# Performance work log

Hardware: AMD Instinct MI355X
Metric: run time of the kernel (lower is better)

Reference implementation:

```python
import jax, jax.numpy as jnp
import numpy as np

C_S, C_Z, H = 384, 128, 8
HD = C_S // H
EPS = 1e-5

def _layernorm(x, g, b):
    mu = jnp.mean(x, axis=-1, keepdims=True)
    var = jnp.mean((x - mu) ** 2, axis=-1, keepdims=True)
    return (x - mu) * jax.lax.rsqrt(var + EPS) * g + b

def setup_inputs() -> dict:
    key = jax.random.key(0)
    ks = jax.random.split(key, 12)
    B, L = 1, 768
    sc = lambda d: 1.0 / np.sqrt(d)
    return {
        "single": jax.random.normal(ks[0], (B, L, C_S), jnp.float32),
        "pair": jax.random.normal(ks[1], (B, L, L, C_Z), jnp.float32),
        "g_s": jnp.ones((C_S,), jnp.float32),
        "b_s": jnp.zeros((C_S,), jnp.float32),
        "g_z": jnp.ones((C_Z,), jnp.float32),
        "b_z": jnp.zeros((C_Z,), jnp.float32),
        "Wq": jax.random.normal(ks[2], (C_S, C_S), jnp.float32) * sc(C_S),
        "Wk": jax.random.normal(ks[3], (C_S, C_S), jnp.float32) * sc(C_S),
        "Wv": jax.random.normal(ks[4], (C_S, C_S), jnp.float32) * sc(C_S),
        "Wb": jax.random.normal(ks[5], (C_Z, H), jnp.float32) * sc(C_Z),
        "Wo": jax.random.normal(ks[6], (C_S, C_S), jnp.float32) * sc(C_S),
        "bo": jnp.zeros((C_S,), jnp.float32),
        "Wg": jax.random.normal(ks[7], (C_S, C_S), jnp.float32) * sc(C_S),
        "bg": jnp.zeros((C_S,), jnp.float32),
    }

def reference(single, pair, g_s, b_s, g_z, b_z, Wq, Wk, Wv, Wb, Wo, bo, Wg, bg):
    B, L, _ = single.shape
    s = _layernorm(single, g_s, b_s)                      # [B,L,C_S]
    z = _layernorm(pair, g_z, b_z)                        # [B,L,L,C_Z]
    q = (s @ Wq.T).reshape(B, L, H, HD)
    k = (s @ Wk.T).reshape(B, L, H, HD)
    v = (s @ Wv.T).reshape(B, L, H, HD)
    attn = jnp.einsum('bihd,bjhd->bhij', q, k) / np.sqrt(HD)
    bias = jnp.einsum('bijz,zh->bhij', z, Wb)             # pair bias per head
    attn = jax.nn.softmax(attn + bias, axis=-1)
    out = jnp.einsum('bhij,bjhd->bihd', attn, v).reshape(B, L, C_S)
    gate = jax.nn.sigmoid(s @ Wg.T + bg)
    return single + gate * (out @ Wo.T + bo)
```

## Files before the change

kernel.cpp:

```cpp
#include <hip/hip_runtime.h>
#include <hip/hip_bf16.h>
#include <cstdint>
#include <cstddef>

#define LSEQ 768
#define CS 384
#define CZ 128
#define NH 8
#define HD 48
#define LL (LSEQ*LSEQ)

static constexpr float EPS = 1e-5f;
static constexpr float QK_SCALE = 0.14433756729740643f;

typedef unsigned short u16;
typedef __attribute__((ext_vector_type(8))) short bf16x8;
typedef __attribute__((ext_vector_type(4))) float f32x4;

__device__ __forceinline__ u16 f2bf_s(float f){
  unsigned int u = __float_as_uint(f);
  unsigned int r = u + 0x7fffu + ((u >> 16) & 1u);
  return (u16)(r >> 16);
}

__global__ void k_ln_single(const float* __restrict__ single,
                            const float* __restrict__ g,
                            const float* __restrict__ b,
                            float* __restrict__ s_out){
  const int i = blockIdx.x;
  const int lane = threadIdx.x;
  const float* row = single + i*CS;
  float x[6];
  float sum = 0.f;
#pragma unroll
  for(int e=0;e<6;e++){ x[e] = row[lane + 64*e]; sum += x[e]; }
#pragma unroll
  for(int m=32;m>=1;m>>=1) sum += __shfl_xor(sum, m, 64);
  const float mu = sum * (1.f/CS);
  float vs = 0.f;
#pragma unroll
  for(int e=0;e<6;e++){ float d = x[e]-mu; vs += d*d; }
#pragma unroll
  for(int m=32;m>=1;m>>=1) vs += __shfl_xor(vs, m, 64);
  const float rs = rsqrtf(vs*(1.f/CS) + EPS);
#pragma unroll
  for(int e=0;e<6;e++){
    int c = lane + 64*e;
    s_out[i*CS + c] = (x[e]-mu)*rs*g[c] + b[c];
  }
}

__global__ __launch_bounds__(256,4) void k_pair_bias(
    const float* __restrict__ pair,
    const float* __restrict__ g_z,
    const float* __restrict__ b_z,
    const float* __restrict__ Wb,
    float* __restrict__ bias){
  const int t = threadIdx.x;
  const int lane = t & 63;
  const int wave = t >> 6;
  const int sub  = lane >> 4;
  const int lg   = lane & 15;
  const int z0   = lg*8;

  float wb_r[64], gz[8], bz[8];
#pragma unroll
  for(int zz=0; zz<8; zz++){
    gz[zz] = g_z[z0+zz];
    bz[zz] = b_z[z0+zz];
#pragma unroll
    for(int h=0; h<NH; h++) wb_r[zz*8+h] = Wb[(z0+zz)*NH + h];
  }
  const int hmap = 4*(lg&1) + (lg&2) + ((lg>>2)&1);

  const int ngroups = LL/16;
  for(int gidx = blockIdx.x; gidx < ngroups; gidx += gridDim.x){
    const int r = gidx*16 + wave*4 + sub;
    const float4 u0 = *(const float4*)(pair + (size_t)r*CZ + z0);
    const float4 u1 = *(const float4*)(pair + (size_t)r*CZ + z0 + 4);
    float x[8] = {u0.x,u0.y,u0.z,u0.w,u1.x,u1.y,u1.z,u1.w};
    float sum=0.f, sq=0.f;
#pragma unroll
    for(int e=0;e<8;e++){ sum += x[e]; sq += x[e]*x[e]; }
#pragma unroll
    for(int m=1;m<16;m<<=1){ sum += __shfl_xor(sum,m,64); sq += __shfl_xor(sq,m,64); }
    const float mu = sum*(1.f/CZ);
    const float rs = rsqrtf(sq*(1.f/CZ) - mu*mu + EPS);
    float acc[8];
#pragma unroll
    for(int h=0;h<8;h++) acc[h]=0.f;
#pragma unroll
    for(int e=0;e<8;e++){
      const float zn = (x[e]-mu)*rs*gz[e] + bz[e];
#pragma unroll
      for(int h=0;h<8;h++) acc[h] += zn*wb_r[e*8+h];
    }
    float k1[4];
    {
      const bool hi = lg & 1;
#pragma unroll
      for(int j=0;j<4;j++){
        float send = hi ? acc[j] : acc[j+4];
        float recv = __shfl_xor(send, 1, 64);
        k1[j] = (hi ? acc[j+4] : acc[j]) + recv;
      }
    }
    float k2[2];
    {
      const bool hi = lg & 2;
#pragma unroll
      for(int j=0;j<2;j++){
        float send = hi ? k1[j] : k1[j+2];
        float recv = __shfl_xor(send, 2, 64);
        k2[j] = (hi ? k1[j+2] : k1[j]) + recv;
      }
    }
    float k3;
    {
      const bool hi = lg & 4;
      float send = hi ? k2[0] : k2[1];
      float recv = __shfl_xor(send, 4, 64);
      k3 = (hi ? k2[1] : k2[0]) + recv;
    }
    k3 += __shfl_xor(k3, 8, 64);
    if(lg < 8) bias[(size_t)hmap*LL + r] = k3;
  }
}

__global__ __launch_bounds__(256) void k_qkvg(
    const float* __restrict__ s,
    const float* __restrict__ Wq, const float* __restrict__ Wk,
    const float* __restrict__ Wv, const float* __restrict__ Wg,
    const float* __restrict__ bg,
    u16* __restrict__ qb, u16* __restrict__ kb,
    u16* __restrict__ vT, float* __restrict__ gate){
  const int which = blockIdx.z;
  const float* W = (which==0)?Wq : (which==1)?Wk : (which==2)?Wv : Wg;
  __shared__ float As[16][65];
  __shared__ float Bs[16][65];
  const int t = threadIdx.x;
  const int m0 = blockIdx.x*64;
  const int n0 = blockIdx.y*64;
  const int tx = t & 15, ty = t >> 4;
  float acc[4][4] = {};
  for(int k0=0;k0<CS;k0+=16){
#pragma unroll
    for(int e=0;e<4;e++){
      int idx = t + e*256;
      int kk = idx & 15, mm = idx >> 4;
      As[kk][mm] = s[(m0+mm)*CS + k0 + kk];
      Bs[kk][mm] = W[(n0+mm)*CS + k0 + kk];
    }
    __syncthreads();
#pragma unroll
    for(int kk=0;kk<16;kk++){
      float a[4], bb[4];
#pragma unroll
      for(int rr=0;rr<4;rr++) a[rr]=As[kk][ty+16*rr];
#pragma unroll
      for(int cc=0;cc<4;cc++) bb[cc]=Bs[kk][tx+16*cc];
#pragma unroll
      for(int rr=0;rr<4;rr++)
#pragma unroll
        for(int cc=0;cc<4;cc++) acc[rr][cc] += a[rr]*bb[cc];
    }
    __syncthreads();
  }
#pragma unroll
  for(int rr=0;rr<4;rr++){
    int m = m0 + ty + 16*rr;
#pragma unroll
    for(int cc=0;cc<4;cc++){
      int n = n0 + tx + 16*cc;
      float val = acc[rr][cc];
      if(which==0)      qb[m*CS+n] = f2bf_s(val*QK_SCALE);
      else if(which==1) kb[m*CS+n] = f2bf_s(val);
      else if(which==2) vT[(size_t)n*LSEQ + m] = f2bf_s(val);
      else              gate[m*CS+n] = 1.f/(1.f + __expf(-(val + bg[n])));
    }
  }
}

__global__ __launch_bounds__(256) void k_flash(
    const u16* __restrict__ qb, const u16* __restrict__ kb,
    const u16* __restrict__ vT, const float* __restrict__ bias,
    float* __restrict__ attno){
  const int h  = blockIdx.y;
  const int i0 = blockIdx.x * 16;
  const int t  = threadIdx.x;
  const int w    = t >> 6;
  const int lane = t & 63;
  const int ln   = lane & 15;
  const int quad = lane >> 4;

  __shared__ u16  S_lds[4][16][32];
  __shared__ float O_lds[4][16][48];
  __shared__ float ml_lds[4][2][16];

  const bf16x8 zf = {0,0,0,0,0,0,0,0};

  bf16x8 aq0, aq1;
  {
    const u16* qrow = qb + (size_t)(i0 + ln)*CS + h*HD;
    aq0 = *(const bf16x8*)(qrow + quad*8);
    aq1 = (quad < 2) ? *(const bf16x8*)(qrow + 32 + quad*8) : zf;
  }

  float m_r[4], l_r[4];
  f32x4 o[3];
#pragma unroll
  for(int r=0;r<4;r++){ m_r[r] = -INFINITY; l_r[r] = 0.f; }
#pragma unroll
  for(int db=0;db<3;db++) o[db] = (f32x4){0.f,0.f,0.f,0.f};

  for(int jt=0; jt<6; jt++){
    const int j0 = w*192 + jt*32;
    f32x4 s_f[2];
#pragma unroll
    for(int jb=0;jb<2;jb++){
      const u16* krow = kb + (size_t)(j0 + jb*16 + ln)*CS + h*HD;
      bf16x8 bk0 = *(const bf16x8*)(krow + quad*8);
      bf16x8 bk1 = (quad < 2) ? *(const bf16x8*)(krow + 32 + quad*8) : zf;
      f32x4 acc = (f32x4){0.f,0.f,0.f,0.f};
      acc = __builtin_amdgcn_mfma_f32_16x16x32_bf16(aq0, bk0, acc, 0,0,0);
      acc = __builtin_amdgcn_mfma_f32_16x16x32_bf16(aq1, bk1, acc, 0,0,0);
      s_f[jb] = acc;
    }
    float sv[2][4];
#pragma unroll
    for(int jb=0;jb<2;jb++)
#pragma unroll
      for(int r=0;r<4;r++)
        sv[jb][r] = s_f[jb][r] +
          bias[(size_t)h*LL + (size_t)(i0 + quad*4 + r)*LSEQ + j0 + jb*16 + ln];
    float tmax[4];
#pragma unroll
    for(int r=0;r<4;r++) tmax[r] = fmaxf(sv[0][r], sv[1][r]);
#pragma unroll
    for(int r=0;r<4;r++)
#pragma unroll
      for(int m=1;m<16;m<<=1) tmax[r] = fmaxf(tmax[r], __shfl_xor(tmax[r], m, 64));
    float alpha[4];
#pragma unroll
    for(int r=0;r<4;r++){
      const float mn = fmaxf(m_r[r], tmax[r]);
      alpha[r] = __expf(m_r[r] - mn);
      m_r[r] = mn;
    }
    float p[2][4], tsum[4];
#pragma unroll
    for(int r=0;r<4;r++){
      p[0][r] = __expf(sv[0][r] - m_r[r]);
      p[1][r] = __expf(sv[1][r] - m_r[r]);
      tsum[r] = p[0][r] + p[1][r];
    }
#pragma unroll
    for(int r=0;r<4;r++)
#pragma unroll
      for(int m=1;m<16;m<<=1) tsum[r] += __shfl_xor(tsum[r], m, 64);
#pragma unroll
    for(int r=0;r<4;r++) l_r[r] = l_r[r]*alpha[r] + tsum[r];
#pragma unroll
    for(int db=0;db<3;db++)
#pragma unroll
      for(int r=0;r<4;r++) o[db][r] *= alpha[r];
#pragma unroll
    for(int jb=0;jb<2;jb++)
#pragma unroll
      for(int r=0;r<4;r++) S_lds[w][quad*4+r][jb*16+ln] = f2bf_s(p[jb][r]);
    bf16x8 ap = *(const bf16x8*)&S_lds[w][ln][quad*8];
#pragma unroll
    for(int db=0;db<3;db++){
      bf16x8 bv = *(const bf16x8*)(vT + (size_t)(h*HD + db*16 + ln)*LSEQ + j0 + quad*8);
      o[db] = __builtin_amdgcn_mfma_f32_16x16x32_bf16(ap, bv, o[db], 0,0,0);
    }
  }

#pragma unroll
  for(int db=0;db<3;db++)
#pragma unroll
    for(int r=0;r<4;r++) O_lds[w][quad*4+r][db*16+ln] = o[db][r];
  if(ln == 0){
#pragma unroll
    for(int r=0;r<4;r++){
      ml_lds[w][0][quad*4+r] = m_r[r];
      ml_lds[w][1][quad*4+r] = l_r[r];
    }
  }
  __syncthreads();
#pragma unroll
  for(int e=0;e<3;e++){
    const int idx = t + e*256;
    const int row = idx / 48, d = idx % 48;
    float M = ml_lds[0][0][row];
#pragma unroll
    for(int ww=1;ww<4;ww++) M = fmaxf(M, ml_lds[ww][0][row]);
    float L = 0.f, O = 0.f;
#pragma unroll
    for(int ww=0;ww<4;ww++){
      const float f = __expf(ml_lds[ww][0][row] - M);
      L += ml_lds[ww][1][row] * f;
      O += O_lds[ww][row][d] * f;
    }
    attno[(size_t)(i0+row)*CS + h*HD + d] = O / L;
  }
}

__global__ __launch_bounds__(256) void k_final(
    const float* __restrict__ attno, const float* __restrict__ Wo,
    const float* __restrict__ bo, const float* __restrict__ single,
    const float* __restrict__ gate, float* __restrict__ out){
  __shared__ float As[16][65];
  __shared__ float Bs[16][65];
  const int t = threadIdx.x;
  const int m0 = blockIdx.x*64;
  const int n0 = blockIdx.y*64;
  const int tx = t & 15, ty = t >> 4;
  float acc[4][4] = {};
  for(int k0=0;k0<CS;k0+=16){
#pragma unroll
    for(int e=0;e<4;e++){
      int idx = t + e*256;
      int kk = idx & 15, mm = idx >> 4;
      As[kk][mm] = attno[(m0+mm)*CS + k0 + kk];
      Bs[kk][mm] = Wo[(n0+mm)*CS + k0 + kk];
    }
    __syncthreads();
#pragma unroll
    for(int kk=0;kk<16;kk++){
      float a[4], bb[4];
#pragma unroll
      for(int rr=0;rr<4;rr++) a[rr]=As[kk][ty+16*rr];
#pragma unroll
      for(int cc=0;cc<4;cc++) bb[cc]=Bs[kk][tx+16*cc];
#pragma unroll
      for(int rr=0;rr<4;rr++)
#pragma unroll
        for(int cc=0;cc<4;cc++) acc[rr][cc] += a[rr]*bb[cc];
    }
    __syncthreads();
  }
#pragma unroll
  for(int rr=0;rr<4;rr++){
    int m = m0 + ty + 16*rr;
#pragma unroll
    for(int cc=0;cc<4;cc++){
      int n = n0 + tx + 16*cc;
      float val = acc[rr][cc] + bo[n];
      out[m*CS+n] = single[m*CS+n] + gate[m*CS+n]*val;
    }
  }
}

extern "C" void kernel_launch(void* const* d_in, const int* in_sizes, int n_in,
                              void* d_out, int out_size, void* d_ws, size_t ws_size,
                              hipStream_t stream){
  (void)in_sizes; (void)n_in; (void)out_size; (void)ws_size;
  const float* single = (const float*)d_in[0];
  const float* pair   = (const float*)d_in[1];
  const float* g_s    = (const float*)d_in[2];
  const float* b_s    = (const float*)d_in[3];
  const float* g_z    = (const float*)d_in[4];
  const float* b_z    = (const float*)d_in[5];
  const float* Wq     = (const float*)d_in[6];
  const float* Wk     = (const float*)d_in[7];
  const float* Wv     = (const float*)d_in[8];
  const float* Wb     = (const float*)d_in[9];
  const float* Wo     = (const float*)d_in[10];
  const float* bo     = (const float*)d_in[11];
  const float* Wg     = (const float*)d_in[12];
  const float* bg     = (const float*)d_in[13];
  float* out = (float*)d_out;

  float* ws     = (float*)d_ws;
  float* bias   = ws;
  float* s      = ws + 4718592;
  float* gate   = s + 294912;
  float* attno  = gate + 294912;
  u16*   qb     = (u16*)(ws + 4718592 + 3*294912);
  u16*   kb     = qb + 294912;
  u16*   vT     = kb + 294912;

  hipLaunchKernelGGL(k_ln_single, dim3(768),     dim3(64),  0, stream, single, g_s, b_s, s);
  hipLaunchKernelGGL(k_pair_bias, dim3(3072),    dim3(256), 0, stream, pair, g_z, b_z, Wb, bias);
  hipLaunchKernelGGL(k_qkvg,      dim3(12,6,4),  dim3(256), 0, stream, s, Wq, Wk, Wv, Wg, bg, qb, kb, vT, gate);
  hipLaunchKernelGGL(k_flash,     dim3(48,8),    dim3(256), 0, stream, qb, kb, vT, bias, attno);
  hipLaunchKernelGGL(k_final,     dim3(12,6),    dim3(256), 0, stream, attno, Wo, bo, single, gate, out);
}
```

Before: 520.4 us.

## Convert projection GEMMs to bf16 MFMA with fused weight/activation conversion

Replaces the scalar fp32 LDS-tiled GEMMs for the QKV/gate and output projections with bf16 16x16x32 MFMA kernels that load operands directly from global memory. A new prep kernel fuses the single-row layernorm with converting all projection weights to bf16. The attention output is also stored as bf16 for the final GEMM. This trades fp32 accuracy in the projections for matrix-core throughput and halved operand traffic, and adds a conversion pass over the weights each call.

```diff
diff --git a/kernel.cpp b/kernel.cpp
--- a/kernel.cpp
+++ b/kernel.cpp
@@ -9,6 +9,7 @@
 #define NH 8
 #define HD 48
 #define LL (LSEQ*LSEQ)
+#define WELEM 147456
 
 static constexpr float EPS = 1e-5f;
 static constexpr float QK_SCALE = 0.14433756729740643f;
@@ -23,30 +24,45 @@
   return (u16)(r >> 16);
 }
 
-__global__ void k_ln_single(const float* __restrict__ single,
-                            const float* __restrict__ g,
-                            const float* __restrict__ b,
-                            float* __restrict__ s_out){
-  const int i = blockIdx.x;
-  const int lane = threadIdx.x;
-  const float* row = single + i*CS;
-  float x[6];
-  float sum = 0.f;
-#pragma unroll
-  for(int e=0;e<6;e++){ x[e] = row[lane + 64*e]; sum += x[e]; }
-#pragma unroll
-  for(int m=32;m>=1;m>>=1) sum += __shfl_xor(sum, m, 64);
-  const float mu = sum * (1.f/CS);
-  float vs = 0.f;
-#pragma unroll
-  for(int e=0;e<6;e++){ float d = x[e]-mu; vs += d*d; }
-#pragma unroll
-  for(int m=32;m>=1;m>>=1) vs += __shfl_xor(vs, m, 64);
-  const float rs = rsqrtf(vs*(1.f/CS) + EPS);
-#pragma unroll
-  for(int e=0;e<6;e++){
-    int c = lane + 64*e;
-    s_out[i*CS + c] = (x[e]-mu)*rs*g[c] + b[c];
+__global__ __launch_bounds__(256) void k_prep(
+    const float* __restrict__ single,
+    const float* __restrict__ g, const float* __restrict__ b,
+    const float* __restrict__ Wq, const float* __restrict__ Wk,
+    const float* __restrict__ Wv, const float* __restrict__ Wg,
+    const float* __restrict__ Wo,
+    u16* __restrict__ s_bf, u16* __restrict__ Wbf){
+  const int blk = blockIdx.x;
+  if(blk < 192){
+    const int wave = threadIdx.x >> 6, lane = threadIdx.x & 63;
+    const int i = blk*4 + wave;
+    const float* row = single + i*CS;
+    float x[6];
+    float sum = 0.f;
+#pragma unroll
+    for(int e=0;e<6;e++){ x[e] = row[lane + 64*e]; sum += x[e]; }
+#pragma unroll
+    for(int m=32;m>=1;m>>=1) sum += __shfl_xor(sum, m, 64);
+    const float mu = sum * (1.f/CS);
+    float vs = 0.f;
+#pragma unroll
+    for(int e=0;e<6;e++){ float d = x[e]-mu; vs += d*d; }
+#pragma unroll
+    for(int m=32;m>=1;m>>=1) vs += __shfl_xor(vs, m, 64);
+    const float rs = rsqrtf(vs*(1.f/CS) + EPS);
+#pragma unroll
+    for(int e=0;e<6;e++){
+      int c = lane + 64*e;
+      s_bf[i*CS + c] = f2bf_s((x[e]-mu)*rs*g[c] + b[c]);
+    }
+  } else {
+    const int idx = (blk-192)*256 + threadIdx.x;
+    const int which = idx / 36864;
+    const int off = (idx - which*36864)*4;
+    const float* src = (which==0)?Wq:(which==1)?Wk:(which==2)?Wv:(which==3)?Wg:Wo;
+    const float4 u = *(const float4*)(src + off);
+    ushort4 o;
+    o.x = f2bf_s(u.x); o.y = f2bf_s(u.y); o.z = f2bf_s(u.z); o.w = f2bf_s(u.w);
+    *(ushort4*)(Wbf + (size_t)which*WELEM + off) = o;
   }
 }
 
@@ -128,55 +144,55 @@
 }
 
 __global__ __launch_bounds__(256) void k_qkvg(
-    const float* __restrict__ s,
-    const float* __restrict__ Wq, const float* __restrict__ Wk,
-    const float* __restrict__ Wv, const float* __restrict__ Wg,
+    const u16* __restrict__ s_bf, const u16* __restrict__ Wbf,
     const float* __restrict__ bg,
     u16* __restrict__ qb, u16* __restrict__ kb,
     u16* __restrict__ vT, float* __restrict__ gate){
-  const int which = blockIdx.z;
-  const float* W = (which==0)?Wq : (which==1)?Wk : (which==2)?Wv : Wg;
-  __shared__ float As[16][65];
-  __shared__ float Bs[16][65];
   const int t = threadIdx.x;
-  const int m0 = blockIdx.x*64;
-  const int n0 = blockIdx.y*64;
-  const int tx = t & 15, ty = t >> 4;
-  float acc[4][4] = {};
-  for(int k0=0;k0<CS;k0+=16){
-#pragma unroll
-    for(int e=0;e<4;e++){
-      int idx = t + e*256;
-      int kk = idx & 15, mm = idx >> 4;
-      As[kk][mm] = s[(m0+mm)*CS + k0 + kk];
-      Bs[kk][mm] = W[(n0+mm)*CS + k0 + kk];
-    }
-    __syncthreads();
-#pragma unroll
-    for(int kk=0;kk<16;kk++){
-      float a[4], bb[4];
-#pragma unroll
-      for(int rr=0;rr<4;rr++) a[rr]=As[kk][ty+16*rr];
-#pragma unroll
-      for(int cc=0;cc<4;cc++) bb[cc]=Bs[kk][tx+16*cc];
-#pragma unroll
-      for(int rr=0;rr<4;rr++)
-#pragma unroll
-        for(int cc=0;cc<4;cc++) acc[rr][cc] += a[rr]*bb[cc];
-    }
-    __syncthreads();
-  }
-#pragma unroll
-  for(int rr=0;rr<4;rr++){
-    int m = m0 + ty + 16*rr;
-#pragma unroll
-    for(int cc=0;cc<4;cc++){
-      int n = n0 + tx + 16*cc;
-      float val = acc[rr][cc];
-      if(which==0)      qb[m*CS+n] = f2bf_s(val*QK_SCALE);
-      else if(which==1) kb[m*CS+n] = f2bf_s(val);
-      else if(which==2) vT[(size_t)n*LSEQ + m] = f2bf_s(val);
-      else              gate[m*CS+n] = 1.f/(1.f + __expf(-(val + bg[n])));
+  const int w = t >> 6, lane = t & 63, ln = lane & 15, quad = lane >> 4;
+  const int m0 = blockIdx.x*64 + w*16;
+  const int which = blockIdx.y / 6;
+  const int n0 = (blockIdx.y % 6)*64;
+  const u16* W = Wbf + (size_t)which*WELEM;
+
+  const u16* arow = s_bf + (size_t)(m0+ln)*CS + quad*8;
+  const u16* brow = W + (size_t)(n0+ln)*CS + quad*8;
+
+  f32x4 acc[4];
+#pragma unroll
+  for(int nb=0;nb<4;nb++) acc[nb] = (f32x4){0.f,0.f,0.f,0.f};
+
+#pragma unroll 4
+  for(int k0=0;k0<CS;k0+=32){
+    bf16x8 a = *(const bf16x8*)(arow + k0);
+#pragma unroll
+    for(int nb=0;nb<4;nb++){
+      bf16x8 bb = *(const bf16x8*)(brow + (size_t)nb*16*CS + k0);
+      acc[nb] = __builtin_amdgcn_mfma_f32_16x16x32_bf16(a, bb, acc[nb], 0,0,0);
+    }
+  }
+
+  if(which == 2){
+#pragma unroll
+    for(int nb=0;nb<4;nb++){
+      const int col = n0 + nb*16 + ln;
+      ushort4 sv;
+      sv.x = f2bf_s(acc[nb][0]); sv.y = f2bf_s(acc[nb][1]);
+      sv.z = f2bf_s(acc[nb][2]); sv.w = f2bf_s(acc[nb][3]);
+      *(ushort4*)(vT + (size_t)col*LSEQ + m0 + quad*4) = sv;
+    }
+  } else {
+#pragma unroll
+    for(int nb=0;nb<4;nb++){
+#pragma unroll
+      for(int r=0;r<4;r++){
+        const int row = m0 + quad*4 + r;
+        const int col = n0 + nb*16 + ln;
+        const float val = acc[nb][r];
+        if(which==0)      qb[row*CS+col] = f2bf_s(val*QK_SCALE);
+        else if(which==1) kb[row*CS+col] = f2bf_s(val);
+        else              gate[row*CS+col] = 1.f/(1.f + __expf(-(val + bg[col])));
+      }
     }
   }
 }
@@ -184,7 +200,7 @@
 __global__ __launch_bounds__(256) void k_flash(
     const u16* __restrict__ qb, const u16* __restrict__ kb,
     const u16* __restrict__ vT, const float* __restrict__ bias,
-    float* __restrict__ attno){
+    u16* __restrict__ attno_bf){
   const int h  = blockIdx.y;
   const int i0 = blockIdx.x * 16;
   const int t  = threadIdx.x;
@@ -302,52 +318,43 @@
       L += ml_lds[ww][1][row] * f;
       O += O_lds[ww][row][d] * f;
     }
-    attno[(size_t)(i0+row)*CS + h*HD + d] = O / L;
+    attno_bf[(size_t)(i0+row)*CS + h*HD + d] = f2bf_s(O / L);
   }
 }
 
 __global__ __launch_bounds__(256) void k_final(
-    const float* __restrict__ attno, const float* __restrict__ Wo,
+    const u16* __restrict__ attno_bf, const u16* __restrict__ Wo_bf,
     const float* __restrict__ bo, const float* __restrict__ single,
     const float* __restrict__ gate, float* __restrict__ out){
-  __shared__ float As[16][65];
-  __shared__ float Bs[16][65];
   const int t = threadIdx.x;
-  const int m0 = blockIdx.x*64;
+  const int w = t >> 6, lane = t & 63, ln = lane & 15, quad = lane >> 4;
+  const int m0 = blockIdx.x*64 + w*16;
   const int n0 = blockIdx.y*64;
-  const int tx = t & 15, ty = t >> 4;
-  float acc[4][4] = {};
-  for(int k0=0;k0<CS;k0+=16){
-#pragma unroll
-    for(int e=0;e<4;e++){
-      int idx = t + e*256;
-      int kk = idx & 15, mm = idx >> 4;
-      As[kk][mm] = attno[(m0+mm)*CS + k0 + kk];
-      Bs[kk][mm] = Wo[(n0+mm)*CS + k0 + kk];
-    }
-    __syncthreads();
-#pragma unroll
-    for(int kk=0;kk<16;kk++){
-      float a[4], bb[4];
-#pragma unroll
-      for(int rr=0;rr<4;rr++) a[rr]=As[kk][ty+16*rr];
-#pragma unroll
-      for(int cc=0;cc<4;cc++) bb[cc]=Bs[kk][tx+16*cc];
-#pragma unroll
-      for(int rr=0;rr<4;rr++)
-#pragma unroll
-        for(int cc=0;cc<4;cc++) acc[rr][cc] += a[rr]*bb[cc];
-    }
-    __syncthreads();
-  }
-#pragma unroll
-  for(int rr=0;rr<4;rr++){
-    int m = m0 + ty + 16*rr;
-#pragma unroll
-    for(int cc=0;cc<4;cc++){
-      int n = n0 + tx + 16*cc;
-      float val = acc[rr][cc] + bo[n];
-      out[m*CS+n] = single[m*CS+n] + gate[m*CS+n]*val;
+
+  const u16* arow = attno_bf + (size_t)(m0+ln)*CS + quad*8;
+  const u16* brow = Wo_bf + (size_t)(n0+ln)*CS + quad*8;
+
+  f32x4 acc[4];
+#pragma unroll
+  for(int nb=0;nb<4;nb++) acc[nb] = (f32x4){0.f,0.f,0.f,0.f};
+
+#pragma unroll 4
+  for(int k0=0;k0<CS;k0+=32){
+    bf16x8 a = *(const bf16x8*)(arow + k0);
+#pragma unroll
+    for(int nb=0;nb<4;nb++){
+      bf16x8 bb = *(const bf16x8*)(brow + (size_t)nb*16*CS + k0);
+      acc[nb] = __builtin_amdgcn_mfma_f32_16x16x32_bf16(a, bb, acc[nb], 0,0,0);
+    }
+  }
+#pragma unroll
+  for(int nb=0;nb<4;nb++){
+#pragma unroll
+    for(int r=0;r<4;r++){
+      const int row = m0 + quad*4 + r;
+      const int col = n0 + nb*16 + ln;
+      const float val = acc[nb][r] + bo[col];
+      out[row*CS+col] = single[row*CS+col] + gate[row*CS+col]*val;
     }
   }
 }
@@ -374,16 +381,20 @@
 
   float* ws     = (float*)d_ws;
   float* bias   = ws;
-  float* s      = ws + 4718592;
-  float* gate   = s + 294912;
-  float* attno  = gate + 294912;
-  u16*   qb     = (u16*)(ws + 4718592 + 3*294912);
+  float* gate   = ws + 4718592;
+  u16*   s_bf   = (u16*)(gate + 294912);
+  u16*   qb     = s_bf + 294912;
   u16*   kb     = qb + 294912;
   u16*   vT     = kb + 294912;
-
-  hipLaunchKernelGGL(k_ln_single, dim3(768),     dim3(64),  0, stream, single, g_s, b_s, s);
-  hipLaunchKernelGGL(k_pair_bias, dim3(3072),    dim3(256), 0, stream, pair, g_z, b_z, Wb, bias);
-  hipLaunchKernelGGL(k_qkvg,      dim3(12,6,4),  dim3(256), 0, stream, s, Wq, Wk, Wv, Wg, bg, qb, kb, vT, gate);
-  hipLaunchKernelGGL(k_flash,     dim3(48,8),    dim3(256), 0, stream, qb, kb, vT, bias, attno);
-  hipLaunchKernelGGL(k_final,     dim3(12,6),    dim3(256), 0, stream, attno, Wo, bo, single, gate, out);
-}
+  u16*   attno  = vT + 294912;
+  u16*   Wbf    = attno + 294912;
+
+  hipLaunchKernelGGL(k_prep,      dim3(912),    dim3(256), 0, stream,
+                     single, g_s, b_s, Wq, Wk, Wv, Wg, Wo, s_bf, Wbf);
+  hipLaunchKernelGGL(k_pair_bias, dim3(3072),   dim3(256), 0, stream, pair, g_z, b_z, Wb, bias);
+  hipLaunchKernelGGL(k_qkvg,      dim3(12,24),  dim3(256), 0, stream,
+                     s_bf, Wbf, bg, qb, kb, vT, gate);
+  hipLaunchKernelGGL(k_flash,     dim3(48,8),   dim3(256), 0, stream, qb, kb, vT, bias, attno);
+  hipLaunchKernelGGL(k_final,     dim3(12,6),   dim3(256), 0, stream,
+                     attno, Wbf + (size_t)4*WELEM, bo, single, gate, out);
+}
```

After: 488.4 us. 6.2% less time.
